# Performance work log

Hardware: AMD Instinct MI355X
Metric: run time of the kernel (lower is better)

Reference implementation:

```python
import jax, jax.numpy as jnp
import numpy as np

N, E, B = 100000, 800000, 64
IN, HC1, HC2, NC, SA = 256, 128, 32, 2, 350
NEG = 0.2  # GATv2Conv default negative_slope


def forward(s_x, s_edge_index, s_batch, s_root_n_id,
            Wq, bq, Wk, bk, Wv, bv,
            Wl1, bl1, Wr1, br1, att1, bias1,
            Wl2, bl2, Wr2, br2, att2, bias2,
            Wl3, bl3, Wr3, br3, att3, bias3,
            c1w, c1b, c2W, c2b, c3W, c3b,
            linW, linb, aW1, ab1, aW2, mW1, mb1, mW2, mb2):
    src, dst = s_edge_index[0], s_edge_index[1]
    x_info = s_x
    # --- SelfAttention over seq_len=1 (x.unsqueeze(1)) ---
    z = s_x[:, None, :]                                   # [N,1,IN]
    q = z @ Wq + bq; k = z @ Wk + bk; v = z @ Wv + bv      # [N,1,SA]
    scores = jnp.einsum('nqd,nkd->nqk', q, k) / jnp.sqrt(jnp.float32(SA))
    probs = jax.nn.softmax(scores, axis=-1)
    h = jnp.einsum('nqk,nkd->nqd', probs, v)[:, 0, :]      # [N,SA]

    def gatv2(x, Wl, bl, Wr, br, att, bias):
        # PyG GATv2Conv, heads=1, eval mode (dropout off)
        xl = x @ Wl + bl                                   # source transform [N,O]
        xr = x @ Wr + br                                   # target transform [N,O]
        e = jax.nn.leaky_relu(xl[src] + xr[dst], NEG)      # [E,O]
        s = e @ att                                        # [E]
        smax = jax.ops.segment_max(s, dst, num_segments=N)
        smax = jnp.where(jnp.isfinite(smax), smax, 0.0)
        ex = jnp.exp(s - smax[dst])
        den = jax.ops.segment_sum(ex, dst, num_segments=N)
        alpha = ex / jnp.maximum(den[dst], 1e-16)
        return jax.ops.segment_sum(alpha[:, None] * xl[src], dst, num_segments=N) + bias

    h = jax.nn.relu(gatv2(h, Wl1, bl1, Wr1, br1, att1, bias1))
    h = jax.nn.relu(gatv2(h, Wl2, bl2, Wr2, br2, att2, bias2))
    h = jax.nn.relu(gatv2(h, Wl3, bl3, Wr3, br3, att3, bias3))   # [N,HC2]

    # --- readout: root node feature ++ global mean pool ---
    cnt = jax.ops.segment_sum(jnp.ones((N,), h.dtype), s_batch, num_segments=B)
    pooled = jax.ops.segment_sum(h, s_batch, num_segments=B) / jnp.maximum(cnt, 1.0)[:, None]
    sx = jnp.concatenate([h[s_root_n_id], pooled], axis=-1)       # [B,2*HC2]

    # --- info branch on raw root features ---
    info = x_info[s_root_n_id]                                    # [B,IN]
    info = c1w[0] * info[:, :-2] + c1w[1] * info[:, 1:-1] + c1w[2] * info[:, 2:] + c1b  # Conv1d(1,1,3)
    t = info.T                                                    # [IN-2,B]
    t = jax.nn.relu(c2W @ t + c2b[:, None])                       # [HC1,B]
    t = jax.nn.relu(c3W @ t + c3b[:, None])                       # [HC1//2,B]
    t = t.T                                                       # [B,HC1//2]
    L = t.shape[1]
    t = jax.nn.relu(t.reshape(B, HC2, L // HC2).mean(-1))         # AdaptiveAvgPool1d(HC2)

    sx = jax.nn.relu(sx @ linW + linb)                            # [B,HC2]

    # --- semantic attention over the two views ---
    emb = jnp.stack([sx, t], axis=1)                              # [B,2,HC2]
    w = jnp.tanh(emb @ aW1 + ab1) @ aW2                           # [B,2,1]
    beta = jax.nn.softmax(w, axis=1)
    emb = (beta * emb).sum(1)                                     # [B,HC2]

    return jax.nn.softmax(jnp.tanh(emb @ mW1 + mb1) @ mW2 + mb2, axis=1)  # [B,NC]


def setup_inputs() -> dict:
    keys = iter(jax.random.split(jax.random.key(0), 64))
    def nrm(*shape):
        return jax.random.normal(next(keys), shape, dtype=jnp.float32) * 0.05
    inp = {}
    inp['s_x'] = jax.random.normal(next(keys), (N, IN), dtype=jnp.float32)
    inp['s_edge_index'] = jax.random.randint(next(keys), (2, E), 0, N)
    inp['s_batch'] = jnp.sort(jax.random.randint(next(keys), (N,), 0, B))
    inp['s_root_n_id'] = jax.random.randint(next(keys), (B,), 0, N)
    inp['Wq'] = nrm(IN, SA); inp['bq'] = nrm(SA)
    inp['Wk'] = nrm(IN, SA); inp['bk'] = nrm(SA)
    inp['Wv'] = nrm(IN, SA); inp['bv'] = nrm(SA)
    inp['Wl1'] = nrm(SA, HC1); inp['bl1'] = nrm(HC1)
    inp['Wr1'] = nrm(SA, HC1); inp['br1'] = nrm(HC1)
    inp['att1'] = nrm(HC1); inp['bias1'] = nrm(HC1)
    inp['Wl2'] = nrm(HC1, HC1 // 2); inp['bl2'] = nrm(HC1 // 2)
    inp['Wr2'] = nrm(HC1, HC1 // 2); inp['br2'] = nrm(HC1 // 2)
    inp['att2'] = nrm(HC1 // 2); inp['bias2'] = nrm(HC1 // 2)
    inp['Wl3'] = nrm(HC1 // 2, HC2); inp['bl3'] = nrm(HC2)
    inp['Wr3'] = nrm(HC1 // 2, HC2); inp['br3'] = nrm(HC2)
    inp['att3'] = nrm(HC2); inp['bias3'] = nrm(HC2)
    inp['c1w'] = nrm(3); inp['c1b'] = nrm(1)
    inp['c2W'] = nrm(HC1, IN - 2); inp['c2b'] = nrm(HC1)
    inp['c3W'] = nrm(HC1 // 2, HC1); inp['c3b'] = nrm(HC1 // 2)
    inp['linW'] = nrm(2 * HC2, HC2); inp['linb'] = nrm(HC2)
    inp['aW1'] = nrm(HC2, 16); inp['ab1'] = nrm(16); inp['aW2'] = nrm(16, 1)
    inp['mW1'] = nrm(HC2, 16); inp['mb1'] = nrm(16)
    inp['mW2'] = nrm(16, NC); inp['mb2'] = nrm(NC)
    return inp


def reference(s_x, s_edge_index, s_batch, s_root_n_id,
              Wq, bq, Wk, bk, Wv, bv,
              Wl1, bl1, Wr1, br1, att1, bias1,
              Wl2, bl2, Wr2, br2, att2, bias2,
              Wl3, bl3, Wr3, br3, att3, bias3,
              c1w, c1b, c2W, c2b, c3W, c3b,
              linW, linb, aW1, ab1, aW2, mW1, mb1, mW2, mb2):
    return forward(s_x, s_edge_index, s_batch, s_root_n_id,
                   Wq, bq, Wk, bk, Wv, bv,
                   Wl1, bl1, Wr1, br1, att1, bias1,
                   Wl2, bl2, Wr2, br2, att2, bias2,
                   Wl3, bl3, Wr3, br3, att3, bias3,
                   c1w, c1b, c2W, c2b, c3W, c3b,
                   linW, linb, aW1, ab1, aW2, mW1, mb1, mW2, mb2)
```

## Files before the change

kernel.cpp:

```cpp
#include <hip/hip_runtime.h>
#include <hip/hip_bf16.h>
#include <math.h>

typedef unsigned short ushort_t;
typedef __attribute__((ext_vector_type(8))) short bfrag;
typedef __attribute__((ext_vector_type(4))) float ffrag;

constexpr int N_NODES = 100000;
constexpr int N_EDGES = 800000;
constexpr int NB      = 64;
constexpr int IN_F    = 256;
constexpr int HC1C    = 128;
constexpr int HC2C    = 32;
constexpr int SA_D    = 350;
constexpr float NEG   = 0.2f;

constexpr int SCAN_NBLK = (N_NODES + 255) / 256;
constexpr int MB64      = (N_NODES + 63) / 64;

constexpr size_t OFF_WT1    = 0;
constexpr size_t OFF_WT2    = OFF_WT1 + 65536;
constexpr size_t OFF_WT3    = OFF_WT2 + 16384;
constexpr size_t OFF_BC1    = OFF_WT3 + 4096;
constexpr size_t OFF_BC2    = OFF_BC1 + 256;
constexpr size_t OFF_BC3    = OFF_BC2 + 128;
constexpr size_t OFF_XLR    = OFF_BC3 + 64;
constexpr size_t OFF_H      = OFF_XLR + (size_t)N_NODES * 256;
constexpr size_t OFF_DEG    = OFF_H + (size_t)N_NODES * 128;
constexpr size_t OFF_ROWPTR = OFF_DEG + N_NODES;
constexpr size_t OFF_CURSOR = OFF_ROWPTR + N_NODES + 1;
constexpr size_t OFF_BLKS   = OFF_CURSOR + N_NODES;
constexpr size_t OFF_BLKO   = OFF_BLKS + 512;
constexpr size_t OFF_CSRSRC = OFF_BLKO + 512;
constexpr size_t OFF_POOLED = OFF_CSRSRC + N_EDGES;
constexpr size_t OFF_CNT    = OFF_POOLED + NB * HC2C;
constexpr size_t WS_FLOATS  = OFF_CNT + NB;

__device__ __forceinline__ ushort_t f2bf(float f) {
  union { float f; unsigned int u; } a;
  a.f = f;
  unsigned int r = a.u + 0x7FFFu + ((a.u >> 16) & 1u);
  return (ushort_t)(r >> 16);
}
__device__ __forceinline__ float bf2f(ushort_t h) {
  union { unsigned int u; float f; } a;
  a.u = ((unsigned int)h) << 16;
  return a.f;
}
__device__ __forceinline__ float2 bfp(unsigned int u) {
  float2 r;
  r.x = __uint_as_float(u << 16);
  r.y = __uint_as_float(u & 0xFFFF0000u);
  return r;
}
__device__ __forceinline__ unsigned int pack2(float a, float b) {
  unsigned int ua = __float_as_uint(a);
  ua += 0x7FFFu + ((ua >> 16) & 1u);
  unsigned int ub = __float_as_uint(b);
  ub += 0x7FFFu + ((ub >> 16) & 1u);
  return __builtin_amdgcn_perm(ub, ua, 0x07060302u);
}
__device__ __forceinline__ void unp8(uint4 u, float* x) {
  float2 p0 = bfp(u.x), p1 = bfp(u.y), p2 = bfp(u.z), p3 = bfp(u.w);
  x[0] = p0.x; x[1] = p0.y; x[2] = p1.x; x[3] = p1.y;
  x[4] = p2.x; x[5] = p2.y; x[6] = p3.x; x[7] = p3.y;
}

__global__ void k_pack_all(const float* __restrict__ Wv, const float* __restrict__ bv,
                           const float* __restrict__ Wl1, const float* __restrict__ bl1,
                           const float* __restrict__ Wr1, const float* __restrict__ br1,
                           const float* __restrict__ Wl2, const float* __restrict__ bl2,
                           const float* __restrict__ Wr2, const float* __restrict__ br2,
                           const float* __restrict__ Wl3, const float* __restrict__ bl3,
                           const float* __restrict__ Wr3, const float* __restrict__ br3,
                           ushort_t* __restrict__ WT1, float* __restrict__ bc1,
                           ushort_t* __restrict__ WT2, float* __restrict__ bc2,
                           ushort_t* __restrict__ WT3, float* __restrict__ bc3) {
  int blk = blockIdx.x;
  int tid = threadIdx.x;
  if (blk < 256) {
    int t = blk * 256 + tid;
    int n = t & 255, k = t >> 8;
    const float* Wx = (n < 128) ? Wl1 : Wr1;
    int j = n & 127;
    float a = 0.f;
    for (int kk = 0; kk < SA_D; ++kk) a += Wv[k * SA_D + kk] * Wx[kk * 128 + j];
    WT1[(size_t)n * 256 + k] = f2bf(a);
  } else if (blk == 256) {
    int n = tid;
    const float* Wx = (n < 128) ? Wl1 : Wr1;
    const float* bx = (n < 128) ? bl1 : br1;
    int j = n & 127;
    float a = bx[j];
    for (int kk = 0; kk < SA_D; ++kk) a += bv[kk] * Wx[kk * 128 + j];
    bc1[n] = a;
  } else if (blk < 321) {
    int t = (blk - 257) * 256 + tid;
    int n = t & 127, k = t >> 7;
    if (t < 128) bc2[t] = (t < 64) ? bl2[t] : br2[t - 64];
    float v = (n < 64) ? Wl2[k * 64 + n] : Wr2[k * 64 + (n - 64)];
    WT2[(size_t)n * 128 + k] = f2bf(v);
  } else {
    int t = (blk - 321) * 256 + tid;
    int n = t & 63, k = t >> 6;
    if (t < 64) bc3[t] = (t < 32) ? bl3[t] : br3[t - 32];
    float v = (n < 32) ? Wl3[k * 32 + n] : Wr3[k * 32 + (n - 32)];
    WT3[(size_t)n * 64 + k] = f2bf(v);
  }
}

__global__ void k_hist(const int* __restrict__ dst, int* __restrict__ deg) {
  int e = blockIdx.x * blockDim.x + threadIdx.x;
  if (e < N_EDGES) atomicAdd(deg + dst[e], 1);
}

__global__ void k_scan_local(const int* __restrict__ deg, int* __restrict__ row_ptr,
                             int* __restrict__ blk_sum) {
  __shared__ int sh[256];
  int t = threadIdx.x;
  int i = blockIdx.x * 256 + t;
  int v = (i < N_NODES) ? deg[i] : 0;
  sh[t] = v;
  __syncthreads();
  for (int off = 1; off < 256; off <<= 1) {
    int add = (t >= off) ? sh[t - off] : 0;
    __syncthreads();
    sh[t] += add;
    __syncthreads();
  }
  if (i < N_NODES) row_ptr[i] = sh[t] - v;
  if (t == 255) blk_sum[blockIdx.x] = sh[255];
}

__global__ void k_scan_blk(const int* __restrict__ blk_sum, int* __restrict__ blk_off) {
  __shared__ int sh[512];
  int t = threadIdx.x;
  int v = (t < SCAN_NBLK) ? blk_sum[t] : 0;
  sh[t] = v;
  __syncthreads();
  for (int off = 1; off < 512; off <<= 1) {
    int add = (t >= off) ? sh[t - off] : 0;
    __syncthreads();
    sh[t] += add;
    __syncthreads();
  }
  blk_off[t] = sh[t] - v;
}

__global__ void k_scan_add(int* __restrict__ row_ptr, const int* __restrict__ blk_off,
                           int* __restrict__ cursor) {
  int i = blockIdx.x * blockDim.x + threadIdx.x;
  if (i < N_NODES) {
    int v = row_ptr[i] + blk_off[i >> 8];
    row_ptr[i] = v;
    cursor[i] = v;
  }
  if (i == 0) row_ptr[N_NODES] = N_EDGES;
}

__global__ void k_fill(const int* __restrict__ src, const int* __restrict__ dst,
                       int* __restrict__ cursor, int* __restrict__ csr_src) {
  int e = blockIdx.x * blockDim.x + threadIdx.x;
  if (e >= N_EDGES) return;
  int pos = atomicAdd(cursor + dst[e], 1);
  csr_src[pos] = src[e];
}

template <int K, int NN, int BN, bool AF32>
__global__ __launch_bounds__(256, 4) void k_gemm_bf16(const void* __restrict__ xin,
                                                      const ushort_t* __restrict__ WT,
                                                      const float* __restrict__ bc,
                                                      ushort_t* __restrict__ out, int M) {
  constexpr int RT  = 2;
  constexpr int CT  = BN / 32;
  constexpr int NK  = K / 32;
  constexpr int BGT = BN / 64;
  constexpr int BUS = 2048 + BN * 32;
  __shared__ __align__(16) ushort_t lds[2][BUS];

  const int tid  = threadIdx.x;
  const int wave = tid >> 6;
  const int lane = tid & 63;
  const int quad = lane >> 4;
  const int l16  = lane & 15;
  const int wrow = wave >> 1;
  const int wcol = wave & 1;
  const int m0   = blockIdx.x * 64;
  const int n0   = blockIdx.y * BN;

  const float*    af32 = (const float*)xin;
  const ushort_t* ab16 = (const ushort_t*)xin;

  const int aline = tid >> 3, alg = tid & 7;
  const int arow  = aline * 2 + (alg >> 2);
  int am = m0 + arow;
  if (am >= M) am = M - 1;
  const size_t aoff = (size_t)am * K + (alg & 3) * 8;
  const int awi = aline * 64 + ((alg ^ (aline & 7)) * 8);

  size_t boff[BGT];
  int    bwi[BGT];
#pragma unroll
  for (int g = 0; g < BGT; ++g) {
    const int sB = g * 256 + tid;
    const int bline = sB >> 3, blg = sB & 7;
    const int brow = bline * 2 + (blg >> 2);
    boff[g] = (size_t)(n0 + brow) * K + (blg & 3) * 8;
    bwi[g]  = 2048 + bline * 64 + ((blg ^ (bline & 7)) * 8);
  }

  int ard[RT];
#pragma unroll
  for (int rt = 0; rt < RT; ++rt) {
    const int row = wrow * 32 + rt * 16 + l16;
    const int line = row >> 1;
    ard[rt] = line * 64 + ((((row & 1) * 4 + quad) ^ (line & 7)) * 8);
  }
  int brd[CT];
#pragma unroll
  for (int ct = 0; ct < CT; ++ct) {
    const int rowb = wcol * (BN / 2) + ct * 16 + l16;
    const int lineb = rowb >> 1;
    brd[ct] = 2048 + lineb * 64 + ((((rowb & 1) * 4 + quad) ^ (lineb & 7)) * 8);
  }

  float4 sf[2][2];
  uint4  sh[2];
  uint4  sb[2][BGT];

  auto LOAD = [&](int ks, int s) {
    if (AF32) {
      sf[s][0] = *(const float4*)(af32 + aoff + (size_t)ks * 32);
      sf[s][1] = *(const float4*)(af32 + aoff + (size_t)ks * 32 + 4);
    } else {
      sh[s] = *(const uint4*)(ab16 + aoff + (size_t)ks * 32);
    }
#pragma unroll
    for (int g = 0; g < BGT; ++g)
      sb[s][g] = *(const uint4*)(WT + boff[g] + (size_t)ks * 32);
  };
  auto WRITE = [&](int s, int b) {
    uint4 w;
    if (AF32) {
      w.x = pack2(sf[s][0].x, sf[s][0].y);
      w.y = pack2(sf[s][0].z, sf[s][0].w);
      w.z = pack2(sf[s][1].x, sf[s][1].y);
      w.w = pack2(sf[s][1].z, sf[s][1].w);
    } else {
      w = sh[s];
    }
    *(uint4*)&lds[b][awi] = w;
#pragma unroll
    for (int g = 0; g < BGT; ++g) *(uint4*)&lds[b][bwi[g]] = sb[s][g];
  };

  ffrag acc[RT][CT];
#pragma unroll
  for (int rt = 0; rt < RT; ++rt)
#pragma unroll
    for (int ct = 0; ct < CT; ++ct) acc[rt][ct] = ffrag{0.f, 0.f, 0.f, 0.f};

  LOAD(0, 0);
  if (NK > 1) LOAD(1, 1);
  WRITE(0, 0);
  __syncthreads();

#pragma unroll
  for (int i = 0; i < NK; ++i) {
    if (i + 2 < NK) LOAD(i + 2, i & 1);
    bfrag a[RT];
#pragma unroll
    for (int rt = 0; rt < RT; ++rt) a[rt] = *(const bfrag*)&lds[i & 1][ard[rt]];
#pragma unroll
    for (int ct = 0; ct < CT; ++ct) {
      bfrag bf = *(const bfrag*)&lds[i & 1][brd[ct]];
#pragma unroll
      for (int rt = 0; rt < RT; ++rt)
        acc[rt][ct] = __builtin_amdgcn_mfma_f32_16x16x32_bf16(a[rt], bf, acc[rt][ct], 0, 0, 0);
    }
    if (i + 1 < NK) {
      WRITE((i + 1) & 1, (i + 1) & 1);
      __syncthreads();
    }
  }

#pragma unroll
  for (int rt = 0; rt < RT; ++rt)
#pragma unroll
    for (int ct = 0; ct < CT; ++ct) {
      const int n = n0 + wcol * (BN / 2) + ct * 16 + l16;
      const float bb = bc[n];
#pragma unroll
      for (int r = 0; r < 4; ++r) {
        const int m = m0 + wrow * 32 + rt * 16 + quad * 4 + r;
        if (m < M) out[(size_t)m * NN + n] = f2bf(acc[rt][ct][r] + bb);
      }
    }
}

template <int C>
__global__ void k_gat(const ushort_t* __restrict__ xlr, const int* __restrict__ row_ptr,
                      const int* __restrict__ csr_src, const float* __restrict__ att,
                      const float* __restrict__ bias, ushort_t* __restrict__ h) {
  constexpr int G = C / 8;
  constexpr int RS = 2 * C;
  int t = blockIdx.x * blockDim.x + threadIdx.x;
  int d = t / G;
  int lane = t - d * G;
  if (d >= N_NODES) return;
  float xr[8], a[8];
  unp8(*(const uint4*)(xlr + (size_t)d * RS + C + lane * 8), xr);
  *(float4*)&a[0] = *(const float4*)(att + lane * 8);
  *(float4*)&a[4] = *(const float4*)(att + lane * 8 + 4);
  float acc[8];
#pragma unroll
  for (int j = 0; j < 8; ++j) acc[j] = 0.f;
  float den = 0.f;
  const int e0 = row_ptr[d], e1 = row_ptr[d + 1];
  int i = e0;
  for (; i + 4 <= e1; i += 4) {
    uint4 u[4];
#pragma unroll
    for (int q = 0; q < 4; ++q)
      u[q] = *(const uint4*)(xlr + (size_t)csr_src[i + q] * RS + lane * 8);
    float xl[4][8];
#pragma unroll
    for (int q = 0; q < 4; ++q) unp8(u[q], xl[q]);
    float p[4] = {0.f, 0.f, 0.f, 0.f};
#pragma unroll
    for (int j = 0; j < 8; ++j) {
#pragma unroll
      for (int q = 0; q < 4; ++q) {
        float v = xl[q][j] + xr[j];
        v = v > 0.f ? v : NEG * v;
        p[q] += a[j] * v;
      }
    }
#pragma unroll
    for (int off = G / 2; off > 0; off >>= 1) {
#pragma unroll
      for (int q = 0; q < 4; ++q) p[q] += __shfl_xor(p[q], off, 64);
    }
    float ex[4];
#pragma unroll
    for (int q = 0; q < 4; ++q) ex[q] = expf(p[q]);
    den += (ex[0] + ex[1]) + (ex[2] + ex[3]);
#pragma unroll
    for (int j = 0; j < 8; ++j)
      acc[j] += (ex[0] * xl[0][j] + ex[1] * xl[1][j]) + (ex[2] * xl[2][j] + ex[3] * xl[3][j]);
  }
  for (; i < e1; ++i) {
    int s = csr_src[i];
    float xl[8];
    unp8(*(const uint4*)(xlr + (size_t)s * RS + lane * 8), xl);
    float p = 0.f;
#pragma unroll
    for (int j = 0; j < 8; ++j) {
      float v = xl[j] + xr[j];
      v = v > 0.f ? v : NEG * v;
      p += a[j] * v;
    }
#pragma unroll
    for (int off = G / 2; off > 0; off >>= 1) p += __shfl_xor(p, off, 64);
    float ex = expf(p);
    den += ex;
#pragma unroll
    for (int j = 0; j < 8; ++j) acc[j] += ex * xl[j];
  }
  float inv = 1.f / fmaxf(den, 1e-16f);
  float o[8];
#pragma unroll
  for (int j = 0; j < 8; ++j)
    o[j] = fmaxf(acc[j] * inv + bias[lane * 8 + j], 0.f);
  uint4 pk;
  pk.x = pack2(o[0], o[1]);
  pk.y = pack2(o[2], o[3]);
  pk.z = pack2(o[4], o[5]);
  pk.w = pack2(o[6], o[7]);
  *(uint4*)(h + (size_t)d * C + lane * 8) = pk;
}

__global__ void k_pool(const ushort_t* __restrict__ h3, const int* __restrict__ batch,
                       float* __restrict__ pooled, float* __restrict__ cnt) {
  constexpr int NPB = 1024;
  constexpr int NPT = NPB / 8;
  int c = threadIdx.x & 31;
  int r = threadIdx.x >> 5;
  int base = blockIdx.x * NPB + r * NPT;
  if (base >= N_NODES) return;
  int end = base + NPT;
  if (end > N_NODES) end = N_NODES;
  int cur_b = batch[base];
  float acc = 0.f, count = 0.f;
  for (int n = base; n < end; ++n) {
    int b = batch[n];
    if (b != cur_b) {
      atomicAdd(pooled + cur_b * HC2C + c, acc);
      if (c == 0) atomicAdd(cnt + cur_b, count);
      cur_b = b;
      acc = 0.f;
      count = 0.f;
    }
    acc += bf2f(h3[(size_t)n * HC2C + c]);
    count += 1.f;
  }
  atomicAdd(pooled + cur_b * HC2C + c, acc);
  if (c == 0) atomicAdd(cnt + cur_b, count);
}

__global__ __launch_bounds__(256) void k_tail(
    const ushort_t* __restrict__ h3, const int* __restrict__ root,
    const float* __restrict__ pooled, const float* __restrict__ cnt,
    const float* __restrict__ linW, const float* __restrict__ linb,
    const float* __restrict__ X, const float* __restrict__ c1w,
    const float* __restrict__ c1b, const float* __restrict__ c2W,
    const float* __restrict__ c2b, const float* __restrict__ c3W,
    const float* __restrict__ c3b, const float* __restrict__ aW1,
    const float* __restrict__ ab1, const float* __restrict__ aW2,
    const float* __restrict__ mW1, const float* __restrict__ mb1,
    const float* __restrict__ mW2, const float* __restrict__ mb2,
    float* __restrict__ out) {
  constexpr int L = IN_F - 2;
  __shared__ float s_info[L];
  __shared__ float s_t1[HC1C];
  __shared__ float s_t2[HC1C / 2];
  __shared__ float s_e0[HC2C];
  __shared__ float s_e1[HC2C];
  const int b = blockIdx.x;
  const int tid = threadIdx.x;
  const int r = root[b];
  const float* xr = X + (size_t)r * IN_F;
  for (int i = tid; i < L; i += 256)
    s_info[i] = c1w[0] * xr[i] + c1w[1] * xr[i + 1] + c1w[2] * xr[i + 2] + c1b[0];
  __syncthreads();
  if (tid < HC1C) {
    float a = c2b[tid];
    for (int i = 0; i < L; ++i) a += c2W[tid * L + i] * s_info[i];
    s_t1[tid] = fmaxf(a, 0.f);
  }
  __syncthreads();
  if (tid < HC1C / 2) {
    float a = c3b[tid];
    for (int i = 0; i < HC1C; ++i) a += c3W[tid * HC1C + i] * s_t1[i];
    s_t2[tid] = fmaxf(a, 0.f);
  }
  __syncthreads();
  if (tid < HC2C) {
    float v = 0.5f * (s_t2[2 * tid] + s_t2[2 * tid + 1]);
    s_e1[tid] = fmaxf(v, 0.f);
  } else if (tid < 2 * HC2C) {
    int j = tid - HC2C;
    float inv = 1.f / fmaxf(cnt[b], 1.f);
    float a = linb[j];
    for (int c = 0; c < HC2C; ++c) a += bf2f(h3[(size_t)r * HC2C + c]) * linW[c * HC2C + j];
    for (int c = 0; c < HC2C; ++c) a += pooled[b * HC2C + c] * inv * linW[(HC2C + c) * HC2C + j];
    s_e0[j] = fmaxf(a, 0.f);
  }
  __syncthreads();
  if (tid == 0) {
    float w0 = 0.f, w1 = 0.f;
    for (int j = 0; j < 16; ++j) {
      float z0 = ab1[j], z1 = ab1[j];
      for (int c = 0; c < HC2C; ++c) {
        z0 += s_e0[c] * aW1[c * 16 + j];
        z1 += s_e1[c] * aW1[c * 16 + j];
      }
      w0 += tanhf(z0) * aW2[j];
      w1 += tanhf(z1) * aW2[j];
    }
    float mx = fmaxf(w0, w1);
    float x0 = expf(w0 - mx), x1 = expf(w1 - mx);
    float inv = 1.f / (x0 + x1);
    float b0 = x0 * inv, b1 = x1 * inv;
    float l0 = mb2[0], l1 = mb2[1];
    for (int j = 0; j < 16; ++j) {
      float z = mb1[j];
      for (int c = 0; c < HC2C; ++c) z += (b0 * s_e0[c] + b1 * s_e1[c]) * mW1[c * 16 + j];
      float tz = tanhf(z);
      l0 += tz * mW2[j * 2 + 0];
      l1 += tz * mW2[j * 2 + 1];
    }
    float m2 = fmaxf(l0, l1);
    float y0 = expf(l0 - m2), y1 = expf(l1 - m2);
    float is = 1.f / (y0 + y1);
    out[b * 2 + 0] = y0 * is;
    out[b * 2 + 1] = y1 * is;
  }
}

extern "C" void kernel_launch(void* const* d_in, const int* in_sizes, int n_in, void* d_out,
                              int out_size, void* d_ws, size_t ws_size, hipStream_t stream) {
  if (ws_size < WS_FLOATS * sizeof(float)) return;

  const float* s_x   = (const float*)d_in[0];
  const int*   edge  = (const int*)d_in[1];
  const int*   batch = (const int*)d_in[2];
  const int*   root  = (const int*)d_in[3];
  const float* Wv    = (const float*)d_in[8];
  const float* bv    = (const float*)d_in[9];
  const float* Wl1   = (const float*)d_in[10];
  const float* bl1   = (const float*)d_in[11];
  const float* Wr1   = (const float*)d_in[12];
  const float* br1   = (const float*)d_in[13];
  const float* att1  = (const float*)d_in[14];
  const float* bias1 = (const float*)d_in[15];
  const float* Wl2   = (const float*)d_in[16];
  const float* bl2   = (const float*)d_in[17];
  const float* Wr2   = (const float*)d_in[18];
  const float* br2   = (const float*)d_in[19];
  const float* att2  = (const float*)d_in[20];
  const float* bias2 = (const float*)d_in[21];
  const float* Wl3   = (const float*)d_in[22];
  const float* bl3   = (const float*)d_in[23];
  const float* Wr3   = (const float*)d_in[24];
  const float* br3   = (const float*)d_in[25];
  const float* att3  = (const float*)d_in[26];
  const float* bias3 = (const float*)d_in[27];
  const float* c1w   = (const float*)d_in[28];
  const float* c1b   = (const float*)d_in[29];
  const float* c2W   = (const float*)d_in[30];
  const float* c2b   = (const float*)d_in[31];
  const float* c3W   = (const float*)d_in[32];
  const float* c3b   = (const float*)d_in[33];
  const float* linW  = (const float*)d_in[34];
  const float* linb  = (const float*)d_in[35];
  const float* aW1   = (const float*)d_in[36];
  const float* ab1   = (const float*)d_in[37];
  const float* aW2   = (const float*)d_in[38];
  const float* mW1   = (const float*)d_in[39];
  const float* mb1   = (const float*)d_in[40];
  const float* mW2   = (const float*)d_in[41];
  const float* mb2   = (const float*)d_in[42];

  const int* src = edge;
  const int* dst = edge + N_EDGES;

  float*    ws      = (float*)d_ws;
  ushort_t* WT1     = (ushort_t*)(ws + OFF_WT1);
  ushort_t* WT2     = (ushort_t*)(ws + OFF_WT2);
  ushort_t* WT3     = (ushort_t*)(ws + OFF_WT3);
  float*    bc1     = ws + OFF_BC1;
  float*    bc2     = ws + OFF_BC2;
  float*    bc3     = ws + OFF_BC3;
  ushort_t* xlr     = (ushort_t*)(ws + OFF_XLR);
  ushort_t* hbuf    = (ushort_t*)(ws + OFF_H);
  int*      deg     = (int*)(ws + OFF_DEG);
  int*      row_ptr = (int*)(ws + OFF_ROWPTR);
  int*      cursor  = (int*)(ws + OFF_CURSOR);
  int*      blks    = (int*)(ws + OFF_BLKS);
  int*      blko    = (int*)(ws + OFF_BLKO);
  int*      csr_src = (int*)(ws + OFF_CSRSRC);
  float*    pooled  = ws + OFF_POOLED;
  float*    cnt     = ws + OFF_CNT;
  float*    out     = (float*)d_out;

  hipMemsetAsync(deg, 0, N_NODES * sizeof(int), stream);
  k_hist<<<(N_EDGES + 255) / 256, 256, 0, stream>>>(dst, deg);
  k_scan_local<<<SCAN_NBLK, 256, 0, stream>>>(deg, row_ptr, blks);
  k_scan_blk<<<1, 512, 0, stream>>>(blks, blko);
  k_scan_add<<<SCAN_NBLK, 256, 0, stream>>>(row_ptr, blko, cursor);
  k_fill<<<(N_EDGES + 255) / 256, 256, 0, stream>>>(src, dst, cursor, csr_src);

  k_pack_all<<<337, 256, 0, stream>>>(Wv, bv, Wl1, bl1, Wr1, br1, Wl2, bl2, Wr2, br2, Wl3,
                                      bl3, Wr3, br3, WT1, bc1, WT2, bc2, WT3, bc3);

  k_gemm_bf16<256, 256, 128, true><<<dim3(MB64, 2), 256, 0, stream>>>(s_x, WT1, bc1, xlr,
                                                                      N_NODES);
  k_gat<128><<<(N_NODES * 16 + 255) / 256, 256, 0, stream>>>(xlr, row_ptr, csr_src, att1,
                                                             bias1, hbuf);

  k_gemm_bf16<128, 128, 128, false><<<dim3(MB64, 1), 256, 0, stream>>>(hbuf, WT2, bc2, xlr,
                                                                       N_NODES);
  k_gat<64><<<(N_NODES * 8 + 255) / 256, 256, 0, stream>>>(xlr, row_ptr, csr_src, att2,
                                                           bias2, hbuf);

  k_gemm_bf16<64, 64, 64, false><<<dim3(MB64, 1), 256, 0, stream>>>(hbuf, WT3, bc3, xlr,
                                                                    N_NODES);
  k_gat<32><<<(N_NODES * 4 + 255) / 256, 256, 0, stream>>>(xlr, row_ptr, csr_src, att3,
                                                           bias3, hbuf);

  hipMemsetAsync(pooled, 0, (NB * HC2C + NB) * sizeof(float), stream);
  k_pool<<<(N_NODES + 1023) / 1024, 256, 0, stream>>>(hbuf, batch, pooled, cnt);
  k_tail<<<NB, 256, 0, stream>>>(hbuf, root, pooled, cnt, linW, linb, s_x, c1w, c1b, c2W,
                                 c2b, c3W, c3b, aW1, ab1, aW2, mW1, mb1, mW2, mb2, out);
}
```

Before: 680.2 us.

## Use direct global-to-LDS loads with triple-buffered pipeline in bf16 GEMM

Replaces the register-staged double-buffered GEMM load path with global_load_lds async copies into a three-stage LDS ring, synchronised through explicit vmcnt waits and raw barriers. For fp32 inputs the bf16 conversion moves from the staging write to the LDS read side, so fp32 tiles are stored in LDS. The goal is to drop register staging and VGPR pressure and to overlap global loads with MFMA work. In exchange it uses more LDS (three buffers, larger A tiles for fp32), which may lower occupancy, and it relies on hand-tuned waitcnt counts being correct.

```diff
diff --git a/kernel.cpp b/kernel.cpp
--- a/kernel.cpp
+++ b/kernel.cpp
@@ -5,6 +5,9 @@
 typedef unsigned short ushort_t;
 typedef __attribute__((ext_vector_type(8))) short bfrag;
 typedef __attribute__((ext_vector_type(4))) float ffrag;
+
+#define GLOBAL_AS __attribute__((address_space(1)))
+#define LDS_AS    __attribute__((address_space(3)))
 
 constexpr int N_NODES = 100000;
 constexpr int N_EDGES = 800000;
@@ -64,6 +67,15 @@
   float2 p0 = bfp(u.x), p1 = bfp(u.y), p2 = bfp(u.z), p3 = bfp(u.w);
   x[0] = p0.x; x[1] = p0.y; x[2] = p1.x; x[3] = p1.y;
   x[4] = p2.x; x[5] = p2.y; x[6] = p3.x; x[7] = p3.y;
+}
+
+template <int N> __device__ __forceinline__ void waitcnt_vm() {
+  if constexpr (N == 0)      asm volatile("s_waitcnt vmcnt(0)" ::: "memory");
+  else if constexpr (N == 1) asm volatile("s_waitcnt vmcnt(1)" ::: "memory");
+  else if constexpr (N == 2) asm volatile("s_waitcnt vmcnt(2)" ::: "memory");
+  else if constexpr (N == 3) asm volatile("s_waitcnt vmcnt(3)" ::: "memory");
+  else if constexpr (N == 4) asm volatile("s_waitcnt vmcnt(4)" ::: "memory");
+  else                       asm volatile("s_waitcnt vmcnt(8)" ::: "memory");
 }
 
 __global__ void k_pack_all(const float* __restrict__ Wv, const float* __restrict__ bv,
@@ -171,18 +183,22 @@
                                                       const ushort_t* __restrict__ WT,
                                                       const float* __restrict__ bc,
                                                       ushort_t* __restrict__ out, int M) {
-  constexpr int RT  = 2;
-  constexpr int CT  = BN / 32;
-  constexpr int NK  = K / 32;
-  constexpr int BGT = BN / 64;
-  constexpr int BUS = 2048 + BN * 32;
-  __shared__ __align__(16) ushort_t lds[2][BUS];
+  constexpr int RT   = 2;
+  constexpr int CT   = BN / 32;
+  constexpr int NK   = K / 32;
+  constexpr int AGI  = AF32 ? 2 : 1;
+  constexpr int BGI  = (BN * 32 * 2 / 16) / 256;
+  constexpr int G    = AGI + BGI;
+  constexpr int AUS  = AF32 ? 4096 : 2048;
+  constexpr int BUFU = AUS + BN * 32;
+  __shared__ __align__(16) ushort_t lds[3][BUFU];
 
   const int tid  = threadIdx.x;
   const int wave = tid >> 6;
   const int lane = tid & 63;
   const int quad = lane >> 4;
   const int l16  = lane & 15;
+  const int x7   = l16 & 7;
   const int wrow = wave >> 1;
   const int wcol = wave & 1;
   const int m0   = blockIdx.x * 64;
@@ -191,68 +207,100 @@
   const float*    af32 = (const float*)xin;
   const ushort_t* ab16 = (const ushort_t*)xin;
 
-  const int aline = tid >> 3, alg = tid & 7;
-  const int arow  = aline * 2 + (alg >> 2);
-  int am = m0 + arow;
-  if (am >= M) am = M - 1;
-  const size_t aoff = (size_t)am * K + (alg & 3) * 8;
-  const int awi = aline * 64 + ((alg ^ (aline & 7)) * 8);
-
-  size_t boff[BGT];
-  int    bwi[BGT];
-#pragma unroll
-  for (int g = 0; g < BGT; ++g) {
-    const int sB = g * 256 + tid;
-    const int bline = sB >> 3, blg = sB & 7;
-    const int brow = bline * 2 + (blg >> 2);
-    boff[g] = (size_t)(n0 + brow) * K + (blg & 3) * 8;
-    bwi[g]  = 2048 + bline * 64 + ((blg ^ (bline & 7)) * 8);
+  size_t aoffs[AGI];
+#pragma unroll
+  for (int it = 0; it < AGI; ++it) {
+    const int s = it * 256 + tid;
+    if (AF32) {
+      const int row = s >> 3;
+      const int g   = (s & 7) ^ (row & 7);
+      int m = m0 + row;
+      if (m >= M) m = M - 1;
+      aoffs[it] = (size_t)m * K + g * 4;
+    } else {
+      const int aline  = s >> 3;
+      const int ainner = (s & 7) ^ (aline & 7);
+      const int arow   = aline * 2 + (ainner >> 2);
+      int m = m0 + arow;
+      if (m >= M) m = M - 1;
+      aoffs[it] = (size_t)m * K + (ainner & 3) * 8;
+    }
+  }
+
+  size_t boff[BGI];
+#pragma unroll
+  for (int g = 0; g < BGI; ++g) {
+    const int s = g * 256 + tid;
+    const int bline  = s >> 3;
+    const int binner = (s & 7) ^ (bline & 7);
+    const int brow   = bline * 2 + (binner >> 2);
+    boff[g] = (size_t)(n0 + brow) * K + (binner & 3) * 8;
   }
 
   int ard[RT];
 #pragma unroll
   for (int rt = 0; rt < RT; ++rt) {
     const int row = wrow * 32 + rt * 16 + l16;
-    const int line = row >> 1;
-    ard[rt] = line * 64 + ((((row & 1) * 4 + quad) ^ (line & 7)) * 8);
+    if (!AF32) {
+      const int line = row >> 1;
+      ard[rt] = line * 64 + ((((row & 1) * 4 + quad) ^ (line & 7)) * 8);
+    } else {
+      ard[rt] = row * 64;
+    }
   }
   int brd[CT];
 #pragma unroll
   for (int ct = 0; ct < CT; ++ct) {
     const int rowb = wcol * (BN / 2) + ct * 16 + l16;
     const int lineb = rowb >> 1;
-    brd[ct] = 2048 + lineb * 64 + ((((rowb & 1) * 4 + quad) ^ (lineb & 7)) * 8);
-  }
-
-  float4 sf[2][2];
-  uint4  sh[2];
-  uint4  sb[2][BGT];
-
-  auto LOAD = [&](int ks, int s) {
-    if (AF32) {
-      sf[s][0] = *(const float4*)(af32 + aoff + (size_t)ks * 32);
-      sf[s][1] = *(const float4*)(af32 + aoff + (size_t)ks * 32 + 4);
-    } else {
-      sh[s] = *(const uint4*)(ab16 + aoff + (size_t)ks * 32);
-    }
-#pragma unroll
-    for (int g = 0; g < BGT; ++g)
-      sb[s][g] = *(const uint4*)(WT + boff[g] + (size_t)ks * 32);
-  };
-  auto WRITE = [&](int s, int b) {
-    uint4 w;
-    if (AF32) {
-      w.x = pack2(sf[s][0].x, sf[s][0].y);
-      w.y = pack2(sf[s][0].z, sf[s][0].w);
-      w.z = pack2(sf[s][1].x, sf[s][1].y);
-      w.w = pack2(sf[s][1].z, sf[s][1].w);
-    } else {
-      w = sh[s];
-    }
-    *(uint4*)&lds[b][awi] = w;
-#pragma unroll
-    for (int g = 0; g < BGT; ++g) *(uint4*)&lds[b][bwi[g]] = sb[s][g];
-  };
+    brd[ct] = AUS + lineb * 64 + ((((rowb & 1) * 4 + quad) ^ (lineb & 7)) * 8);
+  }
+
+#define STAGE(ks, B)                                                        \
+  do {                                                                      \
+    _Pragma("unroll")                                                       \
+    for (int it = 0; it < AGI; ++it) {                                      \
+      const void* asrc = AF32                                               \
+          ? (const void*)(af32 + aoffs[it] + (size_t)(ks) * 32)             \
+          : (const void*)(ab16 + aoffs[it] + (size_t)(ks) * 32);            \
+      __builtin_amdgcn_global_load_lds(                                     \
+          (const GLOBAL_AS unsigned int*)asrc,                              \
+          (LDS_AS unsigned int*)&lds[B][(size_t)((it * 256 + wave * 64) * 8)], \
+          16, 0, 0);                                                        \
+    }                                                                       \
+    _Pragma("unroll")                                                       \
+    for (int g = 0; g < BGI; ++g)                                           \
+      __builtin_amdgcn_global_load_lds(                                     \
+          (const GLOBAL_AS unsigned int*)(WT + boff[g] + (size_t)(ks) * 32),\
+          (LDS_AS unsigned int*)&lds[B][AUS + (size_t)((g * 256 + wave * 64) * 8)], \
+          16, 0, 0);                                                        \
+  } while (0)
+
+#define KSTEP(B)                                                            \
+  do {                                                                      \
+    bfrag a[RT];                                                            \
+    _Pragma("unroll")                                                       \
+    for (int rt = 0; rt < RT; ++rt) {                                       \
+      if (AF32) {                                                           \
+        const float4 u0 = *(const float4*)&lds[B][ard[rt] + (((quad * 2) ^ x7) * 8)]; \
+        const float4 u1 = *(const float4*)&lds[B][ard[rt] + (((quad * 2 + 1) ^ x7) * 8)]; \
+        uint4 d;                                                            \
+        d.x = pack2(u0.x, u0.y);                                            \
+        d.y = pack2(u0.z, u0.w);                                            \
+        d.z = pack2(u1.x, u1.y);                                            \
+        d.w = pack2(u1.z, u1.w);                                            \
+        a[rt] = *(bfrag*)&d;                                                \
+      } else {                                                              \
+        a[rt] = *(const bfrag*)&lds[B][ard[rt]];                            \
+      }                                                                     \
+    }                                                                       \
+    _Pragma("unroll")                                                       \
+    for (int ct = 0; ct < CT; ++ct) {                                       \
+      bfrag bf = *(const bfrag*)&lds[B][brd[ct]];                           \
+      acc[0][ct] = __builtin_amdgcn_mfma_f32_16x16x32_bf16(a[0], bf, acc[0][ct], 0, 0, 0); \
+      acc[1][ct] = __builtin_amdgcn_mfma_f32_16x16x32_bf16(a[1], bf, acc[1][ct], 0, 0, 0); \
+    }                                                                       \
+  } while (0)
 
   ffrag acc[RT][CT];
 #pragma unroll
@@ -260,29 +308,23 @@
 #pragma unroll
     for (int ct = 0; ct < CT; ++ct) acc[rt][ct] = ffrag{0.f, 0.f, 0.f, 0.f};
 
-  LOAD(0, 0);
-  if (NK > 1) LOAD(1, 1);
-  WRITE(0, 0);
-  __syncthreads();
-
-#pragma unroll
-  for (int i = 0; i < NK; ++i) {
-    if (i + 2 < NK) LOAD(i + 2, i & 1);
-    bfrag a[RT];
-#pragma unroll
-    for (int rt = 0; rt < RT; ++rt) a[rt] = *(const bfrag*)&lds[i & 1][ard[rt]];
-#pragma unroll
-    for (int ct = 0; ct < CT; ++ct) {
-      bfrag bf = *(const bfrag*)&lds[i & 1][brd[ct]];
-#pragma unroll
-      for (int rt = 0; rt < RT; ++rt)
-        acc[rt][ct] = __builtin_amdgcn_mfma_f32_16x16x32_bf16(a[rt], bf, acc[rt][ct], 0, 0, 0);
-    }
-    if (i + 1 < NK) {
-      WRITE((i + 1) & 1, (i + 1) & 1);
-      __syncthreads();
-    }
-  }
+  STAGE(0, 0);
+  STAGE(1, 1);
+
+#pragma unroll
+  for (int j = 0; j < NK - 1; ++j) {
+    waitcnt_vm<G>();
+    __builtin_amdgcn_s_barrier();
+    __builtin_amdgcn_sched_barrier(0);
+    if (j + 2 < NK) STAGE(j + 2, (j + 2) % 3);
+    KSTEP(j % 3);
+  }
+  waitcnt_vm<0>();
+  __builtin_amdgcn_s_barrier();
+  __builtin_amdgcn_sched_barrier(0);
+  KSTEP((NK - 1) % 3);
+#undef STAGE
+#undef KSTEP
 
 #pragma unroll
   for (int rt = 0; rt < RT; ++rt)
```

New measurement: 635.8 us. -6.5%, faster.
